# Kernel optimization log

Hardware: AMD Instinct MI355X
Metric: run time of the kernel (lower is better)

## Reference

```python
import jax, jax.numpy as jnp
import numpy as np

N = 20000      # n_nodes
E = 320000     # n_edges (avg degree 16)
DIM = 64       # feature dim
HEADS = 4      # attention heads; per-head channel = DIM (PyG TransformerConv with concat=False)


def setup_inputs() -> dict:
    key = jax.random.key(0)
    ks = jax.random.split(key, 12)
    s = 0.05
    return {
        "f_mole": jax.random.normal(ks[0], (N, DIM), jnp.float32),
        "edge_weight": jax.random.uniform(ks[1], (E,), jnp.float32),
        "gcn_w": jax.random.normal(ks[2], (DIM, DIM), jnp.float32) * s,
        "gcn_b": jnp.zeros((DIM,), jnp.float32),
        "wq": jax.random.normal(ks[3], (DIM, HEADS * DIM), jnp.float32) * s,
        "bq": jnp.zeros((HEADS * DIM,), jnp.float32),
        "wk": jax.random.normal(ks[4], (DIM, HEADS * DIM), jnp.float32) * s,
        "bk": jnp.zeros((HEADS * DIM,), jnp.float32),
        "wv": jax.random.normal(ks[5], (DIM, HEADS * DIM), jnp.float32) * s,
        "bv": jnp.zeros((HEADS * DIM,), jnp.float32),
        "wskip": jax.random.normal(ks[6], (DIM, DIM), jnp.float32) * s,
        "bskip": jnp.zeros((DIM,), jnp.float32),
        "wbeta": jax.random.normal(ks[7], (3 * DIM, 1), jnp.float32) * s,
        "conv_w": jax.random.normal(ks[8], (DIM, DIM), jnp.float32) * s,  # Conv1d weight[o,0,k,0]
        "conv_b": jnp.zeros((DIM,), jnp.float32),
        "edges": jax.random.randint(ks[9], (2, E), 0, N, jnp.int32),
    }


def _forward(f_mole, edge_weight, gcn_w, gcn_b, wq, bq, wk, bk, wv, bv,
             wskip, bskip, wbeta, conv_w, conv_b, edges):
    n = f_mole.shape[0]
    dim = f_mole.shape[1]
    heads = wq.shape[1] // dim
    src, dst = edges[0], edges[1]  # PyG flow: source -> target

    # ---- GCNConv(dim, dim) with edge weights (add_self_loops=True, normalize=True) ----
    loops = jnp.arange(n, dtype=src.dtype)
    src_sl = jnp.concatenate([src, loops])
    dst_sl = jnp.concatenate([dst, loops])
    ew = jnp.concatenate([edge_weight, jnp.ones((n,), f_mole.dtype)])
    deg = jax.ops.segment_sum(ew, dst_sl, num_segments=n)
    dinv = jnp.where(deg > 0, jax.lax.rsqrt(deg), 0.0)
    norm = dinv[src_sl] * ew * dinv[dst_sl]              # (E+N,)
    xw = f_mole @ gcn_w                                   # (N, dim)
    agg = jax.ops.segment_sum(norm[:, None] * xw[src_sl], dst_sl, num_segments=n)
    f_gcn = jax.nn.relu(agg + gcn_b)                      # (N, dim)

    # ---- TransformerConv(dim, dim, heads, concat=False, beta=True) ----
    q = (f_gcn @ wq + bq).reshape(n, heads, dim)
    k = (f_gcn @ wk + bk).reshape(n, heads, dim)
    v = (f_gcn @ wv + bv).reshape(n, heads, dim)
    logits = jnp.einsum('ehc,ehc->eh', q[dst], k[src]) / jnp.sqrt(jnp.float32(dim))  # (E, H)
    m = jax.ops.segment_max(logits, dst, num_segments=n)  # (N, H)
    ex = jnp.exp(logits - m[dst])
    z = jax.ops.segment_sum(ex, dst, num_segments=n)      # (N, H)
    alpha = ex / z[dst]                                   # per-target softmax over edges
    out = jax.ops.segment_sum(alpha[:, :, None] * v[src], dst, num_segments=n)  # (N, H, dim)
    out = out.mean(axis=1)                                # concat=False -> head mean
    x_r = f_gcn @ wskip + bskip                           # root/skip branch
    beta = jax.nn.sigmoid(jnp.concatenate([out, x_r, out - x_r], axis=-1) @ wbeta)  # (N, 1)
    f_tf = jax.nn.relu(beta * x_r + (1.0 - beta) * out)   # (N, dim)

    # ---- Conv1d(1, dim, kernel_size=(dim,1)) on f_tf.T viewed as (1,1,dim,N) ----
    # out[o, n] = sum_k conv_w[o, k] * f_tf.T[k, n] + conv_b[o]  -> shape (1, dim, 1, N)
    conv = jnp.einsum('ok,nk->on', conv_w, f_tf) + conv_b[:, None]  # (dim, N)
    # torch .view(1, n_mole, -1) on (1, dim, 1, N): row-major reshape
    f_intra = conv.reshape(1, n, dim)
    return f_intra


def reference(f_mole, edge_weight, gcn_w, gcn_b, wq, bq, wk, bk, wv, bv,
              wskip, bskip, wbeta, conv_w, conv_b, edges):
    return _forward(f_mole, edge_weight, gcn_w, gcn_b, wq, bq, wk, bk, wv, bv,
                    wskip, bskip, wbeta, conv_w, conv_b, edges)
```

## Files before the change

### kernel.cpp

```cpp
#include <hip/hip_runtime.h>
#include <hip/hip_bf16.h>

#define DIM 64
#define HEADS 4
#define HD 256
#define CAP 64

typedef __attribute__((ext_vector_type(8))) short bf16x8;
typedef __attribute__((ext_vector_type(8))) unsigned short u16x8;
typedef __attribute__((ext_vector_type(4))) float f32x4;

template<int CTRL>
__device__ __forceinline__ float dpp_rot(float x) {
    return __int_as_float(__builtin_amdgcn_update_dpp(
        0, __float_as_int(x), CTRL, 0xF, 0xF, true));
}
__device__ __forceinline__ float reduce16(float x) {
    x += dpp_rot<0x121>(x);
    x += dpp_rot<0x122>(x);
    x += dpp_rot<0x124>(x);
    x += dpp_rot<0x128>(x);
    return x;
}
__device__ __forceinline__ unsigned short f2bf(float f) {
    unsigned u = __float_as_uint(f);
    unsigned r = (u + 0x7FFFu + ((u >> 16) & 1u)) >> 16;
    return (unsigned short)r;
}
__device__ __forceinline__ float bf2f(unsigned short u) {
    return __uint_as_float((unsigned)u << 16);
}

__global__ void scatter_all(const int* __restrict__ edges, const float* __restrict__ ew,
                            int* counts, float* deg, int2* __restrict__ csr, int nE) {
    int e = blockIdx.x * blockDim.x + threadIdx.x;
    if (e < nE) {
        int dst = edges[nE + e];
        int src = edges[e];
        float w = ew[e];
        int p = atomicAdd(&counts[dst], 1);
        int2 rec;
        rec.x = src;
        rec.y = __float_as_int(w);
        csr[(dst << 6) + p] = rec;
        atomicAdd(&deg[dst], w);
    }
}

__device__ __forceinline__ void tile_load_A(float (*As)[68], const float* __restrict__ A,
                                            int row0, int n, int tid) {
    int c4 = (tid & 15) * 4;
    int sw = (tid & 7) << 2;
    #pragma unroll
    for (int it = 0; it < 4; ++it) {
        int r = (tid >> 4) + it * 16;
        float4 val = make_float4(0.f, 0.f, 0.f, 0.f);
        if (row0 + r < n)
            val = *reinterpret_cast<const float4*>(A + (size_t)(row0 + r) * DIM + c4);
        int rs = r ^ sw;
        As[c4 + 0][rs] = val.x;
        As[c4 + 1][rs] = val.y;
        As[c4 + 2][rs] = val.z;
        As[c4 + 3][rs] = val.w;
    }
}

__device__ __forceinline__ void tile_mm(const float (*As)[68], const float (*Bs)[68],
                                        float acc[4][4], int r0, int c0) {
    #pragma unroll 8
    for (int kk = 0; kk < 64; ++kk) {
        int sw = ((kk >> 2) & 7) << 2;
        float4 av = *reinterpret_cast<const float4*>(&As[kk][r0 ^ sw]);
        float4 bv = *reinterpret_cast<const float4*>(&Bs[kk][c0]);
        float a_[4] = {av.x, av.y, av.z, av.w};
        float b_[4] = {bv.x, bv.y, bv.z, bv.w};
        #pragma unroll
        for (int i = 0; i < 4; ++i)
            #pragma unroll
            for (int j = 0; j < 4; ++j)
                acc[i][j] += a_[i] * b_[j];
    }
}

__global__ __launch_bounds__(256) void gemm_xw(const float* __restrict__ A,
                                               const float* __restrict__ W,
                                               const float* __restrict__ deg,
                                               float* __restrict__ dinv,
                                               unsigned short* __restrict__ out,
                                               int n) {
    __shared__ float As[64][68];
    __shared__ float Bs[64][68];
    int row0 = blockIdx.x * 64;
    int tid = threadIdx.x;
    tile_load_A(As, A, row0, n, tid);
    #pragma unroll
    for (int it = 0; it < 4; ++it) {
        int r  = (tid >> 4) + it * 16;
        int c4 = (tid & 15) * 4;
        *reinterpret_cast<float4*>(&Bs[r][c4]) =
            *reinterpret_cast<const float4*>(W + (size_t)r * DIM + c4);
    }
    __syncthreads();
    int r0 = (tid >> 4) * 4;
    int c0 = (tid & 15) * 4;
    float acc[4][4] = {};
    tile_mm(As, Bs, acc, r0, c0);
    #pragma unroll
    for (int i = 0; i < 4; ++i) {
        int r = row0 + r0 + i;
        if (r >= n) continue;
        float d = rsqrtf(deg[r] + 1.0f);
        if (c0 == 0) dinv[r] = d;
        ushort4 u;
        u.x = f2bf(d * acc[i][0]); u.y = f2bf(d * acc[i][1]);
        u.z = f2bf(d * acc[i][2]); u.w = f2bf(d * acc[i][3]);
        *reinterpret_cast<ushort4*>(out + (size_t)r * DIM + c0) = u;
    }
}

__global__ __launch_bounds__(256) void gcn_agg(const unsigned short* __restrict__ xws,
                                               const int* __restrict__ counts,
                                               const int2* __restrict__ csr,
                                               const float* __restrict__ dinv,
                                               const float* __restrict__ gcn_b,
                                               unsigned short* __restrict__ f_gcnh, int n) {
    int wave = threadIdx.x >> 6;
    int lane = threadIdx.x & 63;
    int i = blockIdx.x * 4 + wave;
    if (i >= n) return;
    int eo = lane >> 4;
    int cg = lane & 15;

    float4 acc = make_float4(0.f, 0.f, 0.f, 0.f);
    int e0 = i << 6;
    int e1 = e0 + counts[i];
    int eb = e0;
    for (; eb + 16 <= e1; eb += 16) {
        int2 p[4];
        #pragma unroll
        for (int j = 0; j < 4; ++j) p[j] = csr[eb + 4 * j + eo];
        ushort4 x[4];
        #pragma unroll
        for (int j = 0; j < 4; ++j)
            x[j] = *reinterpret_cast<const ushort4*>(xws + (size_t)p[j].x * DIM + cg * 4);
        #pragma unroll
        for (int j = 0; j < 4; ++j) {
            float c = __int_as_float(p[j].y);
            acc.x += c * bf2f(x[j].x); acc.y += c * bf2f(x[j].y);
            acc.z += c * bf2f(x[j].z); acc.w += c * bf2f(x[j].w);
        }
    }
    for (int e = eb + eo; e < e1; e += 4) {
        int2 p = csr[e];
        float c = __int_as_float(p.y);
        ushort4 x4 = *reinterpret_cast<const ushort4*>(xws + (size_t)p.x * DIM + cg * 4);
        acc.x += c * bf2f(x4.x); acc.y += c * bf2f(x4.y);
        acc.z += c * bf2f(x4.z); acc.w += c * bf2f(x4.w);
    }
    acc.x += __shfl_xor(acc.x, 16, 64); acc.x += __shfl_xor(acc.x, 32, 64);
    acc.y += __shfl_xor(acc.y, 16, 64); acc.y += __shfl_xor(acc.y, 32, 64);
    acc.z += __shfl_xor(acc.z, 16, 64); acc.z += __shfl_xor(acc.z, 32, 64);
    acc.w += __shfl_xor(acc.w, 16, 64); acc.w += __shfl_xor(acc.w, 32, 64);

    float di = dinv[i];
    ushort4 xs = *reinterpret_cast<const ushort4*>(xws + (size_t)i * DIM + cg * 4);
    const float* b = gcn_b + cg * 4;
    if (eo == 0) {
        ushort4 u;
        u.x = f2bf(fmaxf(di * (acc.x + bf2f(xs.x)) + b[0], 0.f));
        u.y = f2bf(fmaxf(di * (acc.y + bf2f(xs.y)) + b[1], 0.f));
        u.z = f2bf(fmaxf(di * (acc.z + bf2f(xs.z)) + b[2], 0.f));
        u.w = f2bf(fmaxf(di * (acc.w + bf2f(xs.w)) + b[3], 0.f));
        *reinterpret_cast<ushort4*>(f_gcnh + (size_t)i * DIM + cg * 4) = u;
    }
}

__global__ __launch_bounds__(256) void qkv_mfma(const unsigned short* __restrict__ Ah,
        const float* __restrict__ wq, const float* __restrict__ bq,
        const float* __restrict__ wk, const float* __restrict__ bk,
        const float* __restrict__ wv, const float* __restrict__ bv,
        const float* __restrict__ wsk, const float* __restrict__ bsk,
        float* __restrict__ qo, unsigned short* __restrict__ kvb,
        float* __restrict__ xrb, int n) {
    int ty = blockIdx.y;
    const float* W; const float* bias; float scale = 1.0f;
    int ncw, mode;
    int col0 = (ty & 3) * 64;
    if (ty < 4)       { W = wq;  bias = bq;  ncw = HD;  mode = 0; scale = 0.125f; }
    else if (ty < 8)  { W = wk;  bias = bk;  ncw = HD;  mode = 1; }
    else if (ty < 12) { W = wv;  bias = bv;  ncw = HD;  mode = 2; }
    else              { W = wsk; bias = bsk; ncw = DIM; mode = 3; col0 = 0; }

    int row0 = blockIdx.x * 64;
    int wid  = threadIdx.x >> 6;
    int lane = threadIdx.x & 63;
    int hm = wid >> 1, hn = wid & 1;
    int lrow = lane & 15;
    int lk8  = (lane >> 4) * 8;

    bf16x8 afr[2][2];
    #pragma unroll
    for (int ks = 0; ks < 2; ++ks)
        #pragma unroll
        for (int fm = 0; fm < 2; ++fm) {
            int r = row0 + hm * 32 + fm * 16 + lrow;
            bf16x8 v8;
            if (r < n) {
                v8 = *reinterpret_cast<const bf16x8*>(Ah + (size_t)r * DIM + ks * 32 + lk8);
            } else {
                #pragma unroll
                for (int j = 0; j < 8; ++j) v8[j] = 0;
            }
            afr[ks][fm] = v8;
        }

    bf16x8 bfr[2][2];
    #pragma unroll
    for (int ks = 0; ks < 2; ++ks)
        #pragma unroll
        for (int fn = 0; fn < 2; ++fn) {
            int c = col0 + hn * 32 + fn * 16 + lrow;
            const float* wp = W + (size_t)(ks * 32 + lk8) * ncw + c;
            bf16x8 v8;
            #pragma unroll
            for (int j = 0; j < 8; ++j)
                v8[j] = (short)f2bf(wp[(size_t)j * ncw]);
            bfr[ks][fn] = v8;
        }

    f32x4 zz = {0.f, 0.f, 0.f, 0.f};
    f32x4 acc[2][2] = {{zz, zz}, {zz, zz}};
    #pragma unroll
    for (int ks = 0; ks < 2; ++ks)
        #pragma unroll
        for (int fm = 0; fm < 2; ++fm)
            #pragma unroll
            for (int fn = 0; fn < 2; ++fn)
                acc[fm][fn] = __builtin_amdgcn_mfma_f32_16x16x32_bf16(
                    afr[ks][fm], bfr[ks][fn], acc[fm][fn], 0, 0, 0);

    int drow = (lane >> 4) * 4;
    int dcol = lane & 15;
    #pragma unroll
    for (int fm = 0; fm < 2; ++fm)
        #pragma unroll
        for (int fn = 0; fn < 2; ++fn) {
            int col = col0 + hn * 32 + fn * 16 + dcol;
            float bcol = bias[col];
            #pragma unroll
            for (int r = 0; r < 4; ++r) {
                int row = row0 + hm * 32 + fm * 16 + drow + r;
                if (row >= n) continue;
                float val = (acc[fm][fn][r] + bcol) * scale;
                if (mode == 0) {
                    qo[(size_t)row * HD + col] = val;
                } else if (mode == 3) {
                    xrb[(size_t)row * DIM + col] = val;
                } else {
                    int h = col >> 6, c6 = col & 63;
                    kvb[(size_t)row * 512 + h * 128 + (c6 >> 2) * 8 + (c6 & 3)
                        + (mode == 2 ? 4 : 0)] = f2bf(val);
                }
            }
        }
}

__global__ __launch_bounds__(256, 2) void attn_fused(const float* __restrict__ q,
                                                  const unsigned short* __restrict__ kvb,
                                                  const float* __restrict__ x_r,
                                                  const int* __restrict__ counts,
                                                  const int2* __restrict__ csr,
                                                  const float* __restrict__ wbeta,
                                                  float* __restrict__ f_tf, int n) {
    int wave = threadIdx.x >> 6;
    int lane = threadIdx.x & 63;
    int i = blockIdx.x * 4 + wave;
    if (i >= n) return;
    int h  = lane >> 4;
    int cg = lane & 15;
    int kvoff = h * 128 + cg * 8;

    float4 q4 = *reinterpret_cast<const float4*>(q + (size_t)i * HD + h * DIM + cg * 4);
    float z = 0.f;
    float4 a = make_float4(0.f, 0.f, 0.f, 0.f);

    int e0 = i << 6;
    int cnt = counts[i];
    int e1 = e0 + cnt;
    int e = e0;
    for (; e + 16 <= e1; e += 16) {
        u16x8 kv[16];
        #pragma unroll
        for (int j = 0; j < 16; ++j) {
            int s = csr[e + j].x;
            kv[j] = *reinterpret_cast<const u16x8*>(kvb + (size_t)s * 512 + kvoff);
        }
        #pragma unroll
        for (int j = 0; j < 16; ++j) {
            float p = q4.x * bf2f(kv[j][0]) + q4.y * bf2f(kv[j][1])
                    + q4.z * bf2f(kv[j][2]) + q4.w * bf2f(kv[j][3]);
            p = reduce16(p);
            float ez = __expf(p);
            z += ez;
            a.x += ez * bf2f(kv[j][4]); a.y += ez * bf2f(kv[j][5]);
            a.z += ez * bf2f(kv[j][6]); a.w += ez * bf2f(kv[j][7]);
        }
    }
    for (; e + 4 <= e1; e += 4) {
        u16x8 kv[4];
        #pragma unroll
        for (int j = 0; j < 4; ++j) {
            int s = csr[e + j].x;
            kv[j] = *reinterpret_cast<const u16x8*>(kvb + (size_t)s * 512 + kvoff);
        }
        #pragma unroll
        for (int j = 0; j < 4; ++j) {
            float p = q4.x * bf2f(kv[j][0]) + q4.y * bf2f(kv[j][1])
                    + q4.z * bf2f(kv[j][2]) + q4.w * bf2f(kv[j][3]);
            p = reduce16(p);
            float ez = __expf(p);
            z += ez;
            a.x += ez * bf2f(kv[j][4]); a.y += ez * bf2f(kv[j][5]);
            a.z += ez * bf2f(kv[j][6]); a.w += ez * bf2f(kv[j][7]);
        }
    }
    for (; e < e1; ++e) {
        int s = csr[e].x;
        u16x8 kv = *reinterpret_cast<const u16x8*>(kvb + (size_t)s * 512 + kvoff);
        float p = q4.x * bf2f(kv[0]) + q4.y * bf2f(kv[1])
                + q4.z * bf2f(kv[2]) + q4.w * bf2f(kv[3]);
        p = reduce16(p);
        float ez = __expf(p);
        z += ez;
        a.x += ez * bf2f(kv[4]); a.y += ez * bf2f(kv[5]);
        a.z += ez * bf2f(kv[6]); a.w += ez * bf2f(kv[7]);
    }

    float inv = (cnt > 0) ? 1.0f / z : 0.f;
    float4 o;
    o.x = a.x * inv; o.y = a.y * inv; o.z = a.z * inv; o.w = a.w * inv;
    o.x += __shfl_xor(o.x, 16, 64); o.x += __shfl_xor(o.x, 32, 64);
    o.y += __shfl_xor(o.y, 16, 64); o.y += __shfl_xor(o.y, 32, 64);
    o.z += __shfl_xor(o.z, 16, 64); o.z += __shfl_xor(o.z, 32, 64);
    o.w += __shfl_xor(o.w, 16, 64); o.w += __shfl_xor(o.w, 32, 64);
    o.x *= 0.25f; o.y *= 0.25f; o.z *= 0.25f; o.w *= 0.25f;

    float4 xr4 = *reinterpret_cast<const float4*>(x_r + (size_t)i * DIM + cg * 4);
    const float* w1 = wbeta + cg * 4;
    const float* w2 = wbeta + 64 + cg * 4;
    const float* w3 = wbeta + 128 + cg * 4;
    float t = o.x * w1[0] + o.y * w1[1] + o.z * w1[2] + o.w * w1[3]
            + xr4.x * w2[0] + xr4.y * w2[1] + xr4.z * w2[2] + xr4.w * w2[3]
            + (o.x - xr4.x) * w3[0] + (o.y - xr4.y) * w3[1]
            + (o.z - xr4.z) * w3[2] + (o.w - xr4.w) * w3[3];
    t = reduce16(t);
    float beta = 1.0f / (1.0f + __expf(-t));
    float4 r;
    r.x = fmaxf(beta * xr4.x + (1.0f - beta) * o.x, 0.f);
    r.y = fmaxf(beta * xr4.y + (1.0f - beta) * o.y, 0.f);
    r.z = fmaxf(beta * xr4.z + (1.0f - beta) * o.z, 0.f);
    r.w = fmaxf(beta * xr4.w + (1.0f - beta) * o.w, 0.f);
    if (h == 0)
        *reinterpret_cast<float4*>(f_tf + (size_t)i * DIM + cg * 4) = r;
}

__global__ __launch_bounds__(256) void conv_out_k(const float* __restrict__ f_tf,
                                                  const float* __restrict__ conv_w,
                                                  const float* __restrict__ conv_b,
                                                  float* __restrict__ out, int n) {
    int nn = blockIdx.x * 256 + threadIdx.x;
    int ob = blockIdx.y * 16;
    if (nn >= n) return;
    float4 r4[16];
    #pragma unroll
    for (int j = 0; j < 16; ++j)
        r4[j] = *reinterpret_cast<const float4*>(f_tf + (size_t)nn * DIM + j * 4);
    #pragma unroll
    for (int oo = 0; oo < 16; ++oo) {
        int o = ob + oo;
        const float* wr = conv_w + (size_t)o * DIM;
        float acc = conv_b[o];
        #pragma unroll
        for (int j = 0; j < 16; ++j) {
            acc += r4[j].x * wr[j * 4 + 0] + r4[j].y * wr[j * 4 + 1] +
                   r4[j].z * wr[j * 4 + 2] + r4[j].w * wr[j * 4 + 3];
        }
        out[(size_t)o * n + nn] = acc;
    }
}

extern "C" void kernel_launch(void* const* d_in, const int* in_sizes, int n_in,
                              void* d_out, int out_size, void* d_ws, size_t ws_size,
                              hipStream_t stream) {
    const float* f_mole = (const float*)d_in[0];
    const float* edge_w = (const float*)d_in[1];
    const float* gcn_w  = (const float*)d_in[2];
    const float* gcn_b  = (const float*)d_in[3];
    const float* wq     = (const float*)d_in[4];
    const float* bq     = (const float*)d_in[5];
    const float* wk     = (const float*)d_in[6];
    const float* bk     = (const float*)d_in[7];
    const float* wv     = (const float*)d_in[8];
    const float* bv     = (const float*)d_in[9];
    const float* wskip  = (const float*)d_in[10];
    const float* bskip  = (const float*)d_in[11];
    const float* wbeta  = (const float*)d_in[12];
    const float* conv_w = (const float*)d_in[13];
    const float* conv_b = (const float*)d_in[14];
    const int*   edges  = (const int*)d_in[15];

    int N = in_sizes[0] / DIM;
    int E = in_sizes[1];

    float* ws = (float*)d_ws;
    size_t o = 0;
    int*   counts  = (int*)(ws + o); o += N;
    float* deg     = ws + o;         o += N;
    float* dinv    = ws + o;         o += N;
    int2*  csr     = (int2*)(ws + o); o += (size_t)2 * N * CAP;
    unsigned short* xws    = (unsigned short*)(ws + o); o += (size_t)N * DIM / 2;
    unsigned short* f_gcnh = (unsigned short*)(ws + o); o += (size_t)N * DIM / 2;
    float* qb      = ws + o;         o += (size_t)N * HD;
    unsigned short* kvb = (unsigned short*)(ws + o); o += (size_t)N * 512 / 2;
    float* xrb     = ws + o;         o += (size_t)N * DIM;
    float* ftf     = ws + o;         o += (size_t)N * DIM;

    int ebl = (E + 255) / 256;
    int nbl = (N + 255) / 256;
    int gbl = (N + 63) / 64;

    hipMemsetAsync(d_ws, 0, (size_t)2 * N * sizeof(int), stream);
    scatter_all<<<ebl, 256, 0, stream>>>(edges, edge_w, counts, deg, csr, E);

    gemm_xw<<<gbl, 256, 0, stream>>>(f_mole, gcn_w, deg, dinv, xws, N);
    gcn_agg<<<(N + 3) / 4, 256, 0, stream>>>(xws, counts, csr, dinv, gcn_b, f_gcnh, N);

    qkv_mfma<<<dim3(gbl, 13), 256, 0, stream>>>(f_gcnh, wq, bq, wk, bk, wv, bv,
                                                wskip, bskip, qb, kvb, xrb, N);

    attn_fused<<<(N + 3) / 4, 256, 0, stream>>>(qb, kvb, xrb, counts, csr, wbeta, ftf, N);
    conv_out_k<<<dim3(nbl, 4), 256, 0, stream>>>(ftf, conv_w, conv_b, (float*)d_out, N);
}
```

Measured before the change: 159.4 us.

## Compute degree from CSR, store Q in bf16, restructure attention gather loop

Drops the float atomicAdd for degree in the scatter kernel and adds a small kernel that sums edge weights from each node's CSR bucket to produce dinv. The Q projection is stored as bf16 instead of fp32, halving Q traffic into the attention kernel. The attention edge loop goes from 16-wide to 8-wide batches, with index loads, gathers, dot products and reductions split into separate phases, and the occupancy hint is removed. The costs are an extra kernel launch with a serial per-thread loop over neighbours, and lower Q precision.

```diff
diff --git a/kernel.cpp b/kernel.cpp
--- a/kernel.cpp
+++ b/kernel.cpp
@@ -32,7 +32,7 @@
 }
 
 __global__ void scatter_all(const int* __restrict__ edges, const float* __restrict__ ew,
-                            int* counts, float* deg, int2* __restrict__ csr, int nE) {
+                            int* counts, int2* __restrict__ csr, int nE) {
     int e = blockIdx.x * blockDim.x + threadIdx.x;
     if (e < nE) {
         int dst = edges[nE + e];
@@ -43,8 +43,19 @@
         rec.x = src;
         rec.y = __float_as_int(w);
         csr[(dst << 6) + p] = rec;
-        atomicAdd(&deg[dst], w);
-    }
+    }
+}
+
+__global__ __launch_bounds__(256) void deg_dinv_k(const int* __restrict__ counts,
+                                                  const int2* __restrict__ csr,
+                                                  float* __restrict__ dinv, int n) {
+    int i = blockIdx.x * 256 + threadIdx.x;
+    if (i >= n) return;
+    int c = counts[i];
+    const int2* p = csr + ((size_t)i << 6);
+    float s = 0.f;
+    for (int j = 0; j < c; ++j) s += __int_as_float(p[j].y);
+    dinv[i] = rsqrtf(s + 1.0f);
 }
 
 __device__ __forceinline__ void tile_load_A(float (*As)[68], const float* __restrict__ A,
@@ -84,8 +95,7 @@
 
 __global__ __launch_bounds__(256) void gemm_xw(const float* __restrict__ A,
                                                const float* __restrict__ W,
-                                               const float* __restrict__ deg,
-                                               float* __restrict__ dinv,
+                                               const float* __restrict__ dinv,
                                                unsigned short* __restrict__ out,
                                                int n) {
     __shared__ float As[64][68];
@@ -109,8 +119,7 @@
     for (int i = 0; i < 4; ++i) {
         int r = row0 + r0 + i;
         if (r >= n) continue;
-        float d = rsqrtf(deg[r] + 1.0f);
-        if (c0 == 0) dinv[r] = d;
+        float d = dinv[r];
         ushort4 u;
         u.x = f2bf(d * acc[i][0]); u.y = f2bf(d * acc[i][1]);
         u.z = f2bf(d * acc[i][2]); u.w = f2bf(d * acc[i][3]);
@@ -180,7 +189,7 @@
         const float* __restrict__ wk, const float* __restrict__ bk,
         const float* __restrict__ wv, const float* __restrict__ bv,
         const float* __restrict__ wsk, const float* __restrict__ bsk,
-        float* __restrict__ qo, unsigned short* __restrict__ kvb,
+        unsigned short* __restrict__ qo, unsigned short* __restrict__ kvb,
         float* __restrict__ xrb, int n) {
     int ty = blockIdx.y;
     const float* W; const float* bias; float scale = 1.0f;
@@ -253,7 +262,7 @@
                 if (row >= n) continue;
                 float val = (acc[fm][fn][r] + bcol) * scale;
                 if (mode == 0) {
-                    qo[(size_t)row * HD + col] = val;
+                    qo[(size_t)row * HD + col] = f2bf(val);
                 } else if (mode == 3) {
                     xrb[(size_t)row * DIM + col] = val;
                 } else {
@@ -265,7 +274,7 @@
         }
 }
 
-__global__ __launch_bounds__(256, 2) void attn_fused(const float* __restrict__ q,
+__global__ __launch_bounds__(256) void attn_fused(const unsigned short* __restrict__ q,
                                                   const unsigned short* __restrict__ kvb,
                                                   const float* __restrict__ x_r,
                                                   const int* __restrict__ counts,
@@ -280,7 +289,9 @@
     int cg = lane & 15;
     int kvoff = h * 128 + cg * 8;
 
-    float4 q4 = *reinterpret_cast<const float4*>(q + (size_t)i * HD + h * DIM + cg * 4);
+    ushort4 qv = *reinterpret_cast<const ushort4*>(q + (size_t)i * HD + h * DIM + cg * 4);
+    float4 q4;
+    q4.x = bf2f(qv.x); q4.y = bf2f(qv.y); q4.z = bf2f(qv.z); q4.w = bf2f(qv.w);
     float z = 0.f;
     float4 a = make_float4(0.f, 0.f, 0.f, 0.f);
 
@@ -288,31 +299,37 @@
     int cnt = counts[i];
     int e1 = e0 + cnt;
     int e = e0;
-    for (; e + 16 <= e1; e += 16) {
-        u16x8 kv[16];
-        #pragma unroll
-        for (int j = 0; j < 16; ++j) {
-            int s = csr[e + j].x;
-            kv[j] = *reinterpret_cast<const u16x8*>(kvb + (size_t)s * 512 + kvoff);
-        }
-        #pragma unroll
-        for (int j = 0; j < 16; ++j) {
-            float p = q4.x * bf2f(kv[j][0]) + q4.y * bf2f(kv[j][1])
-                    + q4.z * bf2f(kv[j][2]) + q4.w * bf2f(kv[j][3]);
-            p = reduce16(p);
-            float ez = __expf(p);
+    for (; e + 8 <= e1; e += 8) {
+        int s[8];
+        #pragma unroll
+        for (int j = 0; j < 8; ++j) s[j] = csr[e + j].x;
+        u16x8 kv[8];
+        #pragma unroll
+        for (int j = 0; j < 8; ++j)
+            kv[j] = *reinterpret_cast<const u16x8*>(kvb + (size_t)s[j] * 512 + kvoff);
+        float pl[8];
+        #pragma unroll
+        for (int j = 0; j < 8; ++j)
+            pl[j] = q4.x * bf2f(kv[j][0]) + q4.y * bf2f(kv[j][1])
+                  + q4.z * bf2f(kv[j][2]) + q4.w * bf2f(kv[j][3]);
+        #pragma unroll
+        for (int j = 0; j < 8; ++j) pl[j] = reduce16(pl[j]);
+        #pragma unroll
+        for (int j = 0; j < 8; ++j) {
+            float ez = __expf(pl[j]);
             z += ez;
             a.x += ez * bf2f(kv[j][4]); a.y += ez * bf2f(kv[j][5]);
             a.z += ez * bf2f(kv[j][6]); a.w += ez * bf2f(kv[j][7]);
         }
     }
     for (; e + 4 <= e1; e += 4) {
+        int s[4];
+        #pragma unroll
+        for (int j = 0; j < 4; ++j) s[j] = csr[e + j].x;
         u16x8 kv[4];
         #pragma unroll
-        for (int j = 0; j < 4; ++j) {
-            int s = csr[e + j].x;
-            kv[j] = *reinterpret_cast<const u16x8*>(kvb + (size_t)s * 512 + kvoff);
-        }
+        for (int j = 0; j < 4; ++j)
+            kv[j] = *reinterpret_cast<const u16x8*>(kvb + (size_t)s[j] * 512 + kvoff);
         #pragma unroll
         for (int j = 0; j < 4; ++j) {
             float p = q4.x * bf2f(kv[j][0]) + q4.y * bf2f(kv[j][1])
@@ -415,13 +432,12 @@
     float* ws = (float*)d_ws;
     size_t o = 0;
     int*   counts  = (int*)(ws + o); o += N;
-    float* deg     = ws + o;         o += N;
     float* dinv    = ws + o;         o += N;
     int2*  csr     = (int2*)(ws + o); o += (size_t)2 * N * CAP;
     unsigned short* xws    = (unsigned short*)(ws + o); o += (size_t)N * DIM / 2;
     unsigned short* f_gcnh = (unsigned short*)(ws + o); o += (size_t)N * DIM / 2;
-    float* qb      = ws + o;         o += (size_t)N * HD;
-    unsigned short* kvb = (unsigned short*)(ws + o); o += (size_t)N * 512 / 2;
+    unsigned short* qb     = (unsigned short*)(ws + o); o += (size_t)N * HD / 2;
+    unsigned short* kvb    = (unsigned short*)(ws + o); o += (size_t)N * 512 / 2;
     float* xrb     = ws + o;         o += (size_t)N * DIM;
     float* ftf     = ws + o;         o += (size_t)N * DIM;
 
@@ -429,10 +445,11 @@
     int nbl = (N + 255) / 256;
     int gbl = (N + 63) / 64;
 
-    hipMemsetAsync(d_ws, 0, (size_t)2 * N * sizeof(int), stream);
-    scatter_all<<<ebl, 256, 0, stream>>>(edges, edge_w, counts, deg, csr, E);
-
-    gemm_xw<<<gbl, 256, 0, stream>>>(f_mole, gcn_w, deg, dinv, xws, N);
+    hipMemsetAsync(d_ws, 0, (size_t)N * sizeof(int), stream);
+    scatter_all<<<ebl, 256, 0, stream>>>(edges, edge_w, counts, csr, E);
+    deg_dinv_k<<<nbl, 256, 0, stream>>>(counts, csr, dinv, N);
+
+    gemm_xw<<<gbl, 256, 0, stream>>>(f_mole, gcn_w, dinv, xws, N);
     gcn_agg<<<(N + 3) / 4, 256, 0, stream>>>(xws, counts, csr, dinv, gcn_b, f_gcnh, N);
 
     qkv_mfma<<<dim3(gbl, 13), 256, 0, stream>>>(f_gcnh, wq, bq, wk, bk, wv, bv,
```

After: 143.2 us. 1.11x faster.
